# Kernel optimization log

Measured on AMD Instinct MI355X. Metric: run time of the kernel, lower is better.

## Reference

```python
import jax, jax.numpy as jnp
import numpy as np

N_NODES = 50000
N_EDGES = 800000
N_GRAPHS = 128
NEG_SLOPE = 0.2


def setup_inputs() -> dict:
    key = jax.random.key(0)
    ks = jax.random.split(key, 16)
    feature = jax.random.normal(ks[0], (N_NODES, 10), dtype=jnp.float32)
    src = jax.random.randint(ks[1], (N_EDGES,), 0, N_NODES, dtype=jnp.int32)
    dst = jax.random.randint(ks[2], (N_EDGES,), 0, N_NODES, dtype=jnp.int32)
    graph_ids = jnp.sort(jax.random.randint(ks[3], (N_NODES,), 0, N_GRAPHS, dtype=jnp.int32))
    s = 0.1
    W1 = jax.random.normal(ks[4], (10, 3 * 32), dtype=jnp.float32) * s
    al1 = jax.random.normal(ks[5], (3, 32), dtype=jnp.float32) * s
    ar1 = jax.random.normal(ks[6], (3, 32), dtype=jnp.float32) * s
    W2 = jax.random.normal(ks[7], (96, 3 * 64), dtype=jnp.float32) * s
    al2 = jax.random.normal(ks[8], (3, 64), dtype=jnp.float32) * s
    ar2 = jax.random.normal(ks[9], (3, 64), dtype=jnp.float32) * s
    d1_w = jax.random.normal(ks[10], (192, 64), dtype=jnp.float32) * s
    d1_b = jnp.zeros((64,), dtype=jnp.float32)
    d2_w = jax.random.normal(ks[11], (64, 1), dtype=jnp.float32) * s
    d2_b = jnp.zeros((1,), dtype=jnp.float32)
    return {"feature": feature, "src": src, "dst": dst, "graph_ids": graph_ids,
            "W1": W1, "al1": al1, "ar1": ar1, "W2": W2, "al2": al2, "ar2": ar2,
            "d1_w": d1_w, "d1_b": d1_b, "d2_w": d2_w, "d2_b": d2_b}


def _edge_softmax(e, dst, n_nodes):
    # e: [E, H] unnormalized logits; softmax over incoming edges of each dst node
    m = jax.ops.segment_max(e, dst, num_segments=n_nodes)  # [N, H]
    ex = jnp.exp(e - m[dst])
    s = jax.ops.segment_sum(ex, dst, num_segments=n_nodes)  # [N, H]
    return ex / (s[dst] + 1e-16)


def _gat_layer(x, W, al, ar, src, dst, n_nodes):
    H, D = al.shape
    z = (x @ W).reshape(n_nodes, H, D)                     # [N, H, D]
    el = jnp.einsum('nhd,hd->nh', z, al)                   # [N, H]
    er = jnp.einsum('nhd,hd->nh', z, ar)
    e = jax.nn.leaky_relu(el[src] + er[dst], NEG_SLOPE)    # [E, H]
    a = _edge_softmax(e, dst, n_nodes)                     # [E, H]
    msg = z[src] * a[:, :, None]                           # [E, H, D]
    out = jax.ops.segment_sum(msg, dst, num_segments=n_nodes)
    return out.reshape(n_nodes, H * D)


def reference(feature, src, dst, graph_ids, W1, al1, ar1, W2, al2, ar2, d1_w, d1_b, d2_w, d2_b):
    n = feature.shape[0]
    x1 = jax.nn.relu(_gat_layer(feature, W1, al1, ar1, src, dst, n))  # [N, 96]
    x2 = jax.nn.relu(_gat_layer(x1, W2, al2, ar2, src, dst, n))       # [N, 192]
    # AvgPooling: mean of node features per graph
    sums = jax.ops.segment_sum(x2, graph_ids, num_segments=N_GRAPHS)  # [G, 192]
    cnts = jax.ops.segment_sum(jnp.ones((n,), x2.dtype), graph_ids, num_segments=N_GRAPHS)
    pooled = sums / jnp.maximum(cnts, 1.0)[:, None]
    h = jax.nn.relu(pooled @ d1_w + d1_b)
    return h @ d2_w + d2_b  # [G, 1]
```

## Files before the change

kernel.cpp:

```cpp
#include <hip/hip_runtime.h>
#include <hip/hip_bf16.h>

#define NEG_SLOPE 0.2f

typedef __attribute__((ext_vector_type(8))) short short8v;
typedef __attribute__((ext_vector_type(4))) float f32x4;

__device__ __forceinline__ float wave_max64(float v) {
    for (int o = 32; o; o >>= 1) v = fmaxf(v, __shfl_xor(v, o));
    return v;
}
__device__ __forceinline__ float wave_sum64(float v) {
    for (int o = 32; o; o >>= 1) v += __shfl_xor(v, o);
    return v;
}
__device__ __forceinline__ unsigned short f2bf(float f) {
    unsigned int u = __float_as_uint(f);
    unsigned int r = (u + 0x7fffu + ((u >> 16) & 1u)) >> 16;
    return (unsigned short)r;
}
__device__ __forceinline__ float bf2f(unsigned short u) {
    return __uint_as_float(((unsigned int)u) << 16);
}


__global__ __launch_bounds__(256) void k_hist(const int* __restrict__ dst,
                                              int* __restrict__ deg,
                                              int* __restrict__ rank, int E) {
    int e = blockIdx.x * 256 + threadIdx.x;
    if (e < E) rank[e] = atomicAdd(&deg[dst[e]], 1);
}


__global__ __launch_bounds__(256) void k_scan1(const int* __restrict__ deg,
                                               int* __restrict__ bsum, int n) {
    int idx = blockIdx.x * 256 + threadIdx.x;
    int v = idx < n ? deg[idx] : 0;
    for (int o = 32; o; o >>= 1) v += __shfl_xor(v, o);
    __shared__ int ws[4];
    if ((threadIdx.x & 63) == 0) ws[threadIdx.x >> 6] = v;
    __syncthreads();
    if (threadIdx.x == 0) bsum[blockIdx.x] = ws[0] + ws[1] + ws[2] + ws[3];
}

__global__ __launch_bounds__(256) void k_scan2(const int* __restrict__ bsum,
                                               int* __restrict__ bpre,
                                               int* __restrict__ row_start,
                                               int nb, int n) {
    __shared__ int s[256];
    int t = threadIdx.x;
    int v = t < nb ? bsum[t] : 0;
    s[t] = v;
    __syncthreads();
    for (int o = 1; o < 256; o <<= 1) {
        int u = (t >= o) ? s[t - o] : 0;
        __syncthreads();
        s[t] += u;
        __syncthreads();
    }
    if (t < nb) bpre[t] = s[t] - v;
    if (t == 255) row_start[n] = s[255];
}

__global__ __launch_bounds__(256) void k_scan3(const int* __restrict__ deg,
                                               const int* __restrict__ bpre,
                                               int* __restrict__ row_start, int n) {
    int idx = blockIdx.x * 256 + threadIdx.x;
    int lane = threadIdx.x & 63;
    int w = threadIdx.x >> 6;
    int d = idx < n ? deg[idx] : 0;
    int x = d;
    for (int o = 1; o < 64; o <<= 1) {
        int u = __shfl_up(x, o);
        if (lane >= o) x += u;
    }
    __shared__ int ws[4];
    if (lane == 63) ws[w] = x;
    __syncthreads();
    int add = bpre[blockIdx.x];
    for (int i = 0; i < w; i++) add += ws[i];
    if (idx < n) row_start[idx] = add + x - d;
}


__global__ void k_scatter(const int* __restrict__ dst, const int* __restrict__ src,
                          const int* __restrict__ rank, const int* __restrict__ row_start,
                          int* __restrict__ ssrc, int E) {
    int e = blockIdx.x * blockDim.x + threadIdx.x;
    if (e < E) {
        int d = dst[e];
        ssrc[row_start[d] + rank[e]] = src[e];
    }
}


__global__ __launch_bounds__(256) void k_gemm1(const float* __restrict__ feat,
                                               const float* __restrict__ W1,
                                               const float* __restrict__ al,
                                               const float* __restrict__ ar,
                                               const float* __restrict__ W2,
                                               unsigned short* __restrict__ W2T,
                                               unsigned short* __restrict__ z1,
                                               float4* __restrict__ el1,
                                               float4* __restrict__ er1, int n) {
    for (int idx = blockIdx.x * 256 + threadIdx.x; idx < 96 * 192; idx += gridDim.x * 256) {
        int c = idx / 96, k = idx - c * 96;
        W2T[idx] = f2bf(W2[k * 192 + c]);
    }
    __shared__ float sW[960], sal[96], sar[96];
    for (int i = threadIdx.x; i < 960; i += 256) sW[i] = W1[i];
    for (int i = threadIdx.x; i < 96; i += 256) { sal[i] = al[i]; sar[i] = ar[i]; }
    __syncthreads();
    int nd = blockIdx.x * 256 + threadIdx.x;
    if (nd >= n) return;
    float x[10];
#pragma unroll
    for (int k = 0; k < 10; k++) x[k] = feat[(size_t)nd * 10 + k];
    float el[3] = {0.f, 0.f, 0.f}, er[3] = {0.f, 0.f, 0.f};
#pragma unroll
    for (int h = 0; h < 3; h++) {
#pragma unroll
        for (int d0 = 0; d0 < 32; d0 += 4) {
            ushort4 o;
            unsigned short* op = &o.x;
#pragma unroll
            for (int q = 0; q < 4; q++) {
                int c = h * 32 + d0 + q;
                float acc = 0.f;
#pragma unroll
                for (int k = 0; k < 10; k++) acc += x[k] * sW[k * 96 + c];
                op[q] = f2bf(acc);
                el[h] += acc * sal[c];
                er[h] += acc * sar[c];
            }
            *reinterpret_cast<ushort4*>(&z1[(size_t)nd * 96 + h * 32 + d0]) = o;
        }
    }
    el1[nd] = make_float4(el[0], el[1], el[2], 0.f);
    er1[nd] = make_float4(er[0], er[1], er[2], 0.f);
}


template <int D, int VW>
__global__ __launch_bounds__(256) void k_agg(const unsigned short* __restrict__ z,
                                             const float4* __restrict__ el,
                                             const float4* __restrict__ er,
                                             const int* __restrict__ row_start,
                                             const int* __restrict__ ssrc,
                                             unsigned short* __restrict__ xout, int n) {
    constexpr int H = 3;
    constexpr int HD = H * D;
    constexpr int NL = HD / VW;
    __shared__ float pl[4][272];
    int wid = (blockIdx.x * blockDim.x + threadIdx.x) >> 6;
    int lane = threadIdx.x & 63;
    int w = threadIdx.x >> 6;
    if (wid >= n) return;
    int s0 = row_start[wid];
    int deg = row_start[wid + 1] - s0;
    unsigned short* orow = xout + (size_t)wid * HD;
    if (deg <= 0) {
        if (lane < NL) {
            if constexpr (VW == 2)
                *reinterpret_cast<ushort2*>(orow + VW * lane) = make_ushort2(0, 0);
            else
                *reinterpret_cast<ushort4*>(orow + VW * lane) = make_ushort4(0, 0, 0, 0);
        }
        return;
    }
    float4 erv = er[wid];
    int hh = (VW * lane) / D;
    if (hh >= H) hh = H - 1;

    if (deg <= 64) {
        bool act = lane < deg;
        int sv = act ? ssrc[s0 + lane] : 0;
        float4 elv = el[sv];
        float v0 = elv.x + erv.x; v0 = v0 > 0.f ? v0 : NEG_SLOPE * v0;
        float v1 = elv.y + erv.y; v1 = v1 > 0.f ? v1 : NEG_SLOPE * v1;
        float v2 = elv.z + erv.z; v2 = v2 > 0.f ? v2 : NEG_SLOPE * v2;
        if (!act) { v0 = -3.402823466e38f; v1 = v0; v2 = v0; }
        float m0 = wave_max64(v0), m1 = wave_max64(v1), m2 = wave_max64(v2);
        float p0 = act ? __expf(v0 - m0) : 0.f;
        float p1 = act ? __expf(v1 - m1) : 0.f;
        float p2 = act ? __expf(v2 - m2) : 0.f;
        float i0 = 1.f / (wave_sum64(p0) + 1e-16f);
        float i1 = 1.f / (wave_sum64(p1) + 1e-16f);
        float i2 = 1.f / (wave_sum64(p2) + 1e-16f);
        pl[w][0 * 68 + lane] = p0 * i0;
        pl[w][1 * 68 + lane] = p1 * i1;
        pl[w][2 * 68 + lane] = p2 * i2;
        reinterpret_cast<int*>(&pl[w][204])[lane] = sv * HD;
        const float* pt = &pl[w][hh * 68];
        const int* zt = reinterpret_cast<const int*>(&pl[w][204]);

        int col = VW * (lane < NL ? lane : NL - 1);
        const unsigned short* zc = z + col;
        float acc0 = 0.f, acc1 = 0.f, acc2 = 0.f, acc3 = 0.f;
        int i = 0;
        for (; i + 8 <= deg; i += 8) {
            int zo[8];
#pragma unroll
            for (int j = 0; j < 8; j++) zo[j] = zt[i + j];
            if constexpr (VW == 2) {
                ushort2 r[8];
#pragma unroll
                for (int j = 0; j < 8; j++)
                    r[j] = *reinterpret_cast<const ushort2*>(zc + zo[j]);
#pragma unroll
                for (int j = 0; j < 8; j++) {
                    float a = pt[i + j];
                    acc0 += a * bf2f(r[j].x); acc1 += a * bf2f(r[j].y);
                }
            } else {
                ushort4 r[8];
#pragma unroll
                for (int j = 0; j < 8; j++)
                    r[j] = *reinterpret_cast<const ushort4*>(zc + zo[j]);
#pragma unroll
                for (int j = 0; j < 8; j++) {
                    float a = pt[i + j];
                    acc0 += a * bf2f(r[j].x); acc1 += a * bf2f(r[j].y);
                    acc2 += a * bf2f(r[j].z); acc3 += a * bf2f(r[j].w);
                }
            }
        }
        for (; i < deg; i++) {
            int zo = zt[i];
            float a = pt[i];
            if constexpr (VW == 2) {
                ushort2 zv = *reinterpret_cast<const ushort2*>(zc + zo);
                acc0 += a * bf2f(zv.x); acc1 += a * bf2f(zv.y);
            } else {
                ushort4 zv = *reinterpret_cast<const ushort4*>(zc + zo);
                acc0 += a * bf2f(zv.x); acc1 += a * bf2f(zv.y);
                acc2 += a * bf2f(zv.z); acc3 += a * bf2f(zv.w);
            }
        }
        if (lane < NL) {
            if constexpr (VW == 2) {
                ushort2 o2;
                o2.x = f2bf(fmaxf(acc0, 0.f)); o2.y = f2bf(fmaxf(acc1, 0.f));
                *reinterpret_cast<ushort2*>(orow + col) = o2;
            } else {
                ushort4 o4;
                o4.x = f2bf(fmaxf(acc0, 0.f)); o4.y = f2bf(fmaxf(acc1, 0.f));
                o4.z = f2bf(fmaxf(acc2, 0.f)); o4.w = f2bf(fmaxf(acc3, 0.f));
                *reinterpret_cast<ushort4*>(orow + col) = o4;
            }
        }
    } else {
        float ern[3] = {erv.x, erv.y, erv.z};
        float m[3] = {-3.402823466e38f, -3.402823466e38f, -3.402823466e38f};
        for (int i = lane; i < deg; i += 64) {
            int sv = ssrc[s0 + i];
            float4 elv = el[sv];
            float vv[3] = {elv.x, elv.y, elv.z};
#pragma unroll
            for (int h = 0; h < 3; h++) {
                float v = vv[h] + ern[h];
                v = v > 0.f ? v : NEG_SLOPE * v;
                m[h] = fmaxf(m[h], v);
            }
        }
#pragma unroll
        for (int h = 0; h < 3; h++) m[h] = wave_max64(m[h]);
        float s[3] = {0.f, 0.f, 0.f};
        for (int i = lane; i < deg; i += 64) {
            int sv = ssrc[s0 + i];
            float4 elv = el[sv];
            float vv[3] = {elv.x, elv.y, elv.z};
#pragma unroll
            for (int h = 0; h < 3; h++) {
                float v = vv[h] + ern[h];
                v = v > 0.f ? v : NEG_SLOPE * v;
                s[h] += __expf(v - m[h]);
            }
        }
#pragma unroll
        for (int h = 0; h < 3; h++) s[h] = 1.f / (wave_sum64(s[h]) + 1e-16f);
        constexpr int NC = (HD + 63) / 64;
        float acc[NC];
#pragma unroll
        for (int j = 0; j < NC; j++) acc[j] = 0.f;
        for (int i = 0; i < deg; i++) {
            int sv = ssrc[s0 + i];
            float4 elv = el[sv];
            float vv[3] = {elv.x, elv.y, elv.z};
            float a[3];
#pragma unroll
            for (int h = 0; h < 3; h++) {
                float v = vv[h] + ern[h];
                v = v > 0.f ? v : NEG_SLOPE * v;
                a[h] = __expf(v - m[h]) * s[h];
            }
            const unsigned short* zr = z + (size_t)sv * HD;
#pragma unroll
            for (int j = 0; j < NC; j++) {
                int c = lane + 64 * j;
                if (c < HD) acc[j] += a[c / D] * bf2f(zr[c]);
            }
        }
#pragma unroll
        for (int j = 0; j < NC; j++) {
            int c = lane + 64 * j;
            if (c < HD) orow[c] = f2bf(fmaxf(acc[j], 0.f));
        }
    }
}


__global__ __launch_bounds__(256) void k_gemm2(const unsigned short* __restrict__ x1,
                                               const unsigned short* __restrict__ W2T,
                                               const float* __restrict__ al,
                                               const float* __restrict__ ar,
                                               unsigned short* __restrict__ z2,
                                               float* __restrict__ el2,
                                               float* __restrict__ er2, int n) {
    int w = threadIdx.x >> 6;
    int l = threadIdx.x & 63;
    int q = l >> 4, c16 = l & 15;
    int Ra = blockIdx.x * 64 + w * 16 + c16;
    short8v afr[3];
    if (Ra < n) {
#pragma unroll
        for (int ks = 0; ks < 3; ks++)
            afr[ks] = *reinterpret_cast<const short8v*>(x1 + (size_t)Ra * 96 + ks * 32 + q * 8);
    } else {
#pragma unroll
        for (int ks = 0; ks < 3; ks++)
#pragma unroll
            for (int i = 0; i < 8; i++) afr[ks][i] = 0;
    }
    f32x4 acc[12];
#pragma unroll
    for (int t = 0; t < 12; t++)
#pragma unroll
        for (int r = 0; r < 4; r++) acc[t][r] = 0.f;
#pragma unroll
    for (int t = 0; t < 12; t++) {
        const unsigned short* bp = W2T + (t * 16 + c16) * 96 + q * 8;
#pragma unroll
        for (int ks = 0; ks < 3; ks++) {
            short8v bfr = *reinterpret_cast<const short8v*>(bp + ks * 32);
            acc[t] = __builtin_amdgcn_mfma_f32_16x16x32_bf16(afr[ks], bfr, acc[t], 0, 0, 0);
        }
    }
    int Rq = blockIdx.x * 64 + w * 16 + q * 4;
    float elp[4][3] = {}, erp[4][3] = {};
#pragma unroll
    for (int t = 0; t < 12; t++) {
        int h = t >> 2;
        float alv = al[t * 16 + c16];
        float arv = ar[t * 16 + c16];
#pragma unroll
        for (int r = 0; r < 4; r++) {
            float v = acc[t][r];
            elp[r][h] += v * alv;
            erp[r][h] += v * arv;
            if (Rq + r < n) z2[(size_t)(Rq + r) * 192 + t * 16 + c16] = f2bf(v);
        }
    }
#pragma unroll
    for (int r = 0; r < 4; r++)
#pragma unroll
        for (int h = 0; h < 3; h++)
#pragma unroll
            for (int o = 1; o < 16; o <<= 1) {
                elp[r][h] += __shfl_xor(elp[r][h], o);
                erp[r][h] += __shfl_xor(erp[r][h], o);
            }
    if (c16 == 0) {
#pragma unroll
        for (int r = 0; r < 4; r++)
            if (Rq + r < n) {
#pragma unroll
                for (int h = 0; h < 3; h++) {
                    el2[(Rq + r) * 4 + h] = elp[r][h];
                    er2[(Rq + r) * 4 + h] = erp[r][h];
                }
            }
    }
}


__global__ __launch_bounds__(192) void k_pool(const unsigned short* __restrict__ x2,
                                              const int* __restrict__ gid,
                                              float* __restrict__ gsum, int n) {
    int base = blockIdx.x * 32;
    if (base >= n) return;
    int end = base + 32; if (end > n) end = n;
    int c = threadIdx.x;
    float acc = 0.f;
    int gprev = gid[base];
    for (int i = base; i < end; i++) {
        int g = gid[i];
        if (g != gprev) {
            atomicAdd(&gsum[gprev * 192 + c], acc);
            acc = 0.f;
            gprev = g;
        }
        acc += bf2f(x2[(size_t)i * 192 + c]);
    }
    atomicAdd(&gsum[gprev * 192 + c], acc);
}


__global__ __launch_bounds__(64) void k_head(const float* __restrict__ gsum,
                                             const int* __restrict__ gid,
                                             const float* __restrict__ d1w,
                                             const float* __restrict__ d1b,
                                             const float* __restrict__ d2w,
                                             const float* __restrict__ d2b,
                                             float* __restrict__ out, int n, int G) {
    int g = blockIdx.x, j = threadIdx.x;
    int lo0 = 0, hi0 = n;
    while (lo0 < hi0) { int mid = (lo0 + hi0) >> 1; if (gid[mid] < g) lo0 = mid + 1; else hi0 = mid; }
    int lo1 = lo0, hi1 = n;
    while (lo1 < hi1) { int mid = (lo1 + hi1) >> 1; if (gid[mid] < g + 1) lo1 = mid + 1; else hi1 = mid; }
    float inv = 1.f / fmaxf((float)(lo1 - lo0), 1.f);
    float h = d1b[j];
    for (int k = 0; k < 192; k++) h += (gsum[g * 192 + k] * inv) * d1w[(size_t)k * 64 + j];
    h = fmaxf(h, 0.f);
    float v = h * d2w[j];
    for (int o = 32; o; o >>= 1) v += __shfl_xor(v, o);
    if (j == 0) out[g] = v + d2b[0];
}


extern "C" void kernel_launch(void* const* d_in, const int* in_sizes, int n_in,
                              void* d_out, int out_size, void* d_ws, size_t ws_size,
                              hipStream_t stream) {
    const float* feat = (const float*)d_in[0];
    const int* src = (const int*)d_in[1];
    const int* dst = (const int*)d_in[2];
    const int* gid = (const int*)d_in[3];
    const float* W1 = (const float*)d_in[4];
    const float* al1 = (const float*)d_in[5];
    const float* ar1 = (const float*)d_in[6];
    const float* W2 = (const float*)d_in[7];
    const float* al2 = (const float*)d_in[8];
    const float* ar2 = (const float*)d_in[9];
    const float* d1w = (const float*)d_in[10];
    const float* d1b = (const float*)d_in[11];
    const float* d2w = (const float*)d_in[12];
    const float* d2b = (const float*)d_in[13];
    float* out = (float*)d_out;
    const int N = in_sizes[0] / 10;
    const int E = in_sizes[1];
    const int G = out_size;
    const int NB = (N + 255) / 256;

    char* p = (char*)d_ws;
    auto take = [&](size_t bytes) -> char* {
        char* r = p;
        p += (bytes + 255) & ~(size_t)255;
        return r;
    };
    unsigned short* z1 = (unsigned short*)take((size_t)N * 96 * 2);
    unsigned short* x1 = (unsigned short*)take((size_t)N * 96 * 2);
    unsigned short* x2 = z1;
    unsigned short* z2 = (unsigned short*)take((size_t)N * 192 * 2);
    float4* el1 = (float4*)take((size_t)N * 16);
    float4* er1 = (float4*)take((size_t)N * 16);
    float* el2 = (float*)take((size_t)N * 16);
    float* er2 = (float*)take((size_t)N * 16);
    unsigned short* W2T = (unsigned short*)take((size_t)96 * 192 * 2);
    int* rank = (int*)take((size_t)E * 4);
    int* bsum = (int*)take((size_t)NB * 4);
    int* bpre = (int*)take((size_t)NB * 4);
    size_t zbytes = (size_t)N * 4 + (size_t)G * 192 * 4;
    int* deg = (int*)take(zbytes);
    float* gsum = (float*)(deg + N);
    int* row_start = (int*)take((size_t)(N + 1) * 4);
    int* ssrc = (int*)take((size_t)E * 4);

    hipMemsetAsync(deg, 0, zbytes, stream);

    k_hist<<<(E + 255) / 256, 256, 0, stream>>>(dst, deg, rank, E);
    k_gemm1<<<(N + 255) / 256, 256, 0, stream>>>(feat, W1, al1, ar1, W2, W2T,
                                                 z1, el1, er1, N);
    k_scan1<<<NB, 256, 0, stream>>>(deg, bsum, N);
    k_scan2<<<1, 256, 0, stream>>>(bsum, bpre, row_start, NB, N);
    k_scan3<<<NB, 256, 0, stream>>>(deg, bpre, row_start, N);
    k_scatter<<<(E + 255) / 256, 256, 0, stream>>>(dst, src, rank, row_start, ssrc, E);

    k_agg<32, 2><<<((size_t)N * 64 + 255) / 256, 256, 0, stream>>>(
        z1, el1, er1, row_start, ssrc, x1, N);
    k_gemm2<<<(N + 63) / 64, 256, 0, stream>>>(x1, W2T, al2, ar2, z2, el2, er2, N);
    k_agg<64, 4><<<((size_t)N * 64 + 255) / 256, 256, 0, stream>>>(
        z2, (const float4*)el2, (const float4*)er2, row_start, ssrc, x2, N);
    k_pool<<<(N + 31) / 32, 192, 0, stream>>>(x2, gid, gsum, N);
    k_head<<<G, 64, 0, stream>>>(gsum, gid, d1w, d1b, d2w, d2b, out, N, G);
}
```

Before: 286.8 us.

## Aggregate before projecting in both GAT layers and precompute attention vectors

Uses linearity to reorder each GAT layer: attention logits come from precomputed W·a vectors, so el/er no longer need the projected features. Raw input features (10 per node, per head) are aggregated first and then projected by W1. Layer 2 aggregates 96-wide x1 once per head into a 288-wide buffer and then runs a per-head MFMA GEMM. The aim is to shrink per-edge gather width, since layer 1 gathers 10 floats instead of 96 bf16. The cost is a larger intermediate (y2 at 288 wide) and an extra projection pass.

```diff
diff --git a/kernel.cpp b/kernel.cpp
--- a/kernel.cpp
+++ b/kernel.cpp
@@ -22,13 +22,38 @@
 __device__ __forceinline__ float bf2f(unsigned short u) {
     return __uint_as_float(((unsigned int)u) << 16);
 }
+__device__ __forceinline__ float bflo(unsigned int pk) {
+    return __uint_as_float(pk << 16);
+}
+__device__ __forceinline__ float bfhi(unsigned int pk) {
+    return __uint_as_float(pk & 0xFFFF0000u);
+}
 
 
 __global__ __launch_bounds__(256) void k_hist(const int* __restrict__ dst,
                                               int* __restrict__ deg,
-                                              int* __restrict__ rank, int E) {
-    int e = blockIdx.x * 256 + threadIdx.x;
-    if (e < E) rank[e] = atomicAdd(&deg[dst[e]], 1);
+                                              int* __restrict__ rank, int E,
+                                              const float* __restrict__ W2,
+                                              const float* __restrict__ al2,
+                                              const float* __restrict__ ar2,
+                                              unsigned short* __restrict__ W2T,
+                                              float* __restrict__ val2,
+                                              float* __restrict__ var2) {
+    int idx = blockIdx.x * 256 + threadIdx.x;
+    if (idx < 96 * 192) {
+        int c = idx / 96, k = idx - c * 96;
+        W2T[idx] = f2bf(W2[k * 192 + c]);
+    } else if (idx < 96 * 192 + 2 * 288) {
+        int t = idx - 96 * 192;
+        int which = t / 288;
+        int tt = t - which * 288;
+        int h = tt / 96, j = tt - h * 96;
+        const float* av = which ? ar2 : al2;
+        float a = 0.f;
+        for (int d = 0; d < 64; d++) a += W2[j * 192 + h * 64 + d] * av[h * 64 + d];
+        (which ? var2 : val2)[tt] = a;
+    }
+    if (idx < E) rank[idx] = atomicAdd(&deg[dst[idx]], 1);
 }
 
 
@@ -82,75 +107,60 @@
     if (idx < n) row_start[idx] = add + x - d;
 }
 
-
 __global__ void k_scatter(const int* __restrict__ dst, const int* __restrict__ src,
                           const int* __restrict__ rank, const int* __restrict__ row_start,
                           int* __restrict__ ssrc, int E) {
     int e = blockIdx.x * blockDim.x + threadIdx.x;
-    if (e < E) {
-        int d = dst[e];
-        ssrc[row_start[d] + rank[e]] = src[e];
-    }
-}
-
-
-__global__ __launch_bounds__(256) void k_gemm1(const float* __restrict__ feat,
-                                               const float* __restrict__ W1,
-                                               const float* __restrict__ al,
-                                               const float* __restrict__ ar,
-                                               const float* __restrict__ W2,
-                                               unsigned short* __restrict__ W2T,
-                                               unsigned short* __restrict__ z1,
-                                               float4* __restrict__ el1,
-                                               float4* __restrict__ er1, int n) {
-    for (int idx = blockIdx.x * 256 + threadIdx.x; idx < 96 * 192; idx += gridDim.x * 256) {
-        int c = idx / 96, k = idx - c * 96;
-        W2T[idx] = f2bf(W2[k * 192 + c]);
-    }
-    __shared__ float sW[960], sal[96], sar[96];
+    if (e < E) ssrc[row_start[dst[e]] + rank[e]] = src[e];
+}
+
+
+__global__ __launch_bounds__(256) void k_el1(const float* __restrict__ feat,
+                                             const float* __restrict__ W1,
+                                             const float* __restrict__ al,
+                                             const float* __restrict__ ar,
+                                             float4* __restrict__ el1,
+                                             float4* __restrict__ er1, int n) {
+    __shared__ float sW[960], sal[96], sar[96], sval[30], svar[30];
     for (int i = threadIdx.x; i < 960; i += 256) sW[i] = W1[i];
     for (int i = threadIdx.x; i < 96; i += 256) { sal[i] = al[i]; sar[i] = ar[i]; }
     __syncthreads();
-    int nd = blockIdx.x * 256 + threadIdx.x;
+    int t = threadIdx.x;
+    if (t < 30) {
+        int h = t / 10, k = t - h * 10;
+        float a = 0.f, b = 0.f;
+        for (int d = 0; d < 32; d++) {
+            float wv = sW[k * 96 + h * 32 + d];
+            a += wv * sal[h * 32 + d];
+            b += wv * sar[h * 32 + d];
+        }
+        sval[t] = a; svar[t] = b;
+    }
+    __syncthreads();
+    int nd = blockIdx.x * 256 + t;
     if (nd >= n) return;
     float x[10];
 #pragma unroll
     for (int k = 0; k < 10; k++) x[k] = feat[(size_t)nd * 10 + k];
-    float el[3] = {0.f, 0.f, 0.f}, er[3] = {0.f, 0.f, 0.f};
-#pragma unroll
-    for (int h = 0; h < 3; h++) {
-#pragma unroll
-        for (int d0 = 0; d0 < 32; d0 += 4) {
-            ushort4 o;
-            unsigned short* op = &o.x;
-#pragma unroll
-            for (int q = 0; q < 4; q++) {
-                int c = h * 32 + d0 + q;
-                float acc = 0.f;
-#pragma unroll
-                for (int k = 0; k < 10; k++) acc += x[k] * sW[k * 96 + c];
-                op[q] = f2bf(acc);
-                el[h] += acc * sal[c];
-                er[h] += acc * sar[c];
-            }
-            *reinterpret_cast<ushort4*>(&z1[(size_t)nd * 96 + h * 32 + d0]) = o;
-        }
-    }
+    float el[3] = {}, er[3] = {};
+#pragma unroll
+    for (int h = 0; h < 3; h++)
+#pragma unroll
+        for (int k = 0; k < 10; k++) {
+            el[h] += x[k] * sval[h * 10 + k];
+            er[h] += x[k] * svar[h * 10 + k];
+        }
     el1[nd] = make_float4(el[0], el[1], el[2], 0.f);
     er1[nd] = make_float4(er[0], er[1], er[2], 0.f);
 }
 
 
-template <int D, int VW>
-__global__ __launch_bounds__(256) void k_agg(const unsigned short* __restrict__ z,
-                                             const float4* __restrict__ el,
-                                             const float4* __restrict__ er,
-                                             const int* __restrict__ row_start,
-                                             const int* __restrict__ ssrc,
-                                             unsigned short* __restrict__ xout, int n) {
-    constexpr int H = 3;
-    constexpr int HD = H * D;
-    constexpr int NL = HD / VW;
+__global__ __launch_bounds__(256) void k_agg1(const float* __restrict__ feat,
+                                              const float4* __restrict__ el,
+                                              const float4* __restrict__ er,
+                                              const int* __restrict__ row_start,
+                                              const int* __restrict__ ssrc,
+                                              float* __restrict__ y1, int n) {
     __shared__ float pl[4][272];
     int wid = (blockIdx.x * blockDim.x + threadIdx.x) >> 6;
     int lane = threadIdx.x & 63;
@@ -158,19 +168,14 @@
     if (wid >= n) return;
     int s0 = row_start[wid];
     int deg = row_start[wid + 1] - s0;
-    unsigned short* orow = xout + (size_t)wid * HD;
     if (deg <= 0) {
-        if (lane < NL) {
-            if constexpr (VW == 2)
-                *reinterpret_cast<ushort2*>(orow + VW * lane) = make_ushort2(0, 0);
-            else
-                *reinterpret_cast<ushort4*>(orow + VW * lane) = make_ushort4(0, 0, 0, 0);
-        }
+        if (lane < 30) y1[(size_t)wid * 30 + lane] = 0.f;
         return;
     }
     float4 erv = er[wid];
-    int hh = (VW * lane) / D;
-    if (hh >= H) hh = H - 1;
+    int ll = lane & 31, hf = lane >> 5;
+    int h = ll / 10, k = ll - (ll / 10) * 10;
+    if (ll >= 30) { h = 2; k = 9; }
 
     if (deg <= 64) {
         bool act = lane < deg;
@@ -190,65 +195,33 @@
         pl[w][0 * 68 + lane] = p0 * i0;
         pl[w][1 * 68 + lane] = p1 * i1;
         pl[w][2 * 68 + lane] = p2 * i2;
-        reinterpret_cast<int*>(&pl[w][204])[lane] = sv * HD;
-        const float* pt = &pl[w][hh * 68];
+        reinterpret_cast<int*>(&pl[w][204])[lane] = sv * 10;
+        const float* pt = &pl[w][h * 68];
         const int* zt = reinterpret_cast<const int*>(&pl[w][204]);
 
-        int col = VW * (lane < NL ? lane : NL - 1);
-        const unsigned short* zc = z + col;
-        float acc0 = 0.f, acc1 = 0.f, acc2 = 0.f, acc3 = 0.f;
+        float acc = 0.f;
         int i = 0;
         for (; i + 8 <= deg; i += 8) {
-            int zo[8];
-#pragma unroll
-            for (int j = 0; j < 8; j++) zo[j] = zt[i + j];
-            if constexpr (VW == 2) {
-                ushort2 r[8];
-#pragma unroll
-                for (int j = 0; j < 8; j++)
-                    r[j] = *reinterpret_cast<const ushort2*>(zc + zo[j]);
-#pragma unroll
-                for (int j = 0; j < 8; j++) {
-                    float a = pt[i + j];
-                    acc0 += a * bf2f(r[j].x); acc1 += a * bf2f(r[j].y);
-                }
-            } else {
-                ushort4 r[8];
-#pragma unroll
-                for (int j = 0; j < 8; j++)
-                    r[j] = *reinterpret_cast<const ushort4*>(zc + zo[j]);
-#pragma unroll
-                for (int j = 0; j < 8; j++) {
-                    float a = pt[i + j];
-                    acc0 += a * bf2f(r[j].x); acc1 += a * bf2f(r[j].y);
-                    acc2 += a * bf2f(r[j].z); acc3 += a * bf2f(r[j].w);
-                }
-            }
-        }
-        for (; i < deg; i++) {
-            int zo = zt[i];
-            float a = pt[i];
-            if constexpr (VW == 2) {
-                ushort2 zv = *reinterpret_cast<const ushort2*>(zc + zo);
-                acc0 += a * bf2f(zv.x); acc1 += a * bf2f(zv.y);
-            } else {
-                ushort4 zv = *reinterpret_cast<const ushort4*>(zc + zo);
-                acc0 += a * bf2f(zv.x); acc1 += a * bf2f(zv.y);
-                acc2 += a * bf2f(zv.z); acc3 += a * bf2f(zv.w);
-            }
-        }
-        if (lane < NL) {
-            if constexpr (VW == 2) {
-                ushort2 o2;
-                o2.x = f2bf(fmaxf(acc0, 0.f)); o2.y = f2bf(fmaxf(acc1, 0.f));
-                *reinterpret_cast<ushort2*>(orow + col) = o2;
-            } else {
-                ushort4 o4;
-                o4.x = f2bf(fmaxf(acc0, 0.f)); o4.y = f2bf(fmaxf(acc1, 0.f));
-                o4.z = f2bf(fmaxf(acc2, 0.f)); o4.w = f2bf(fmaxf(acc3, 0.f));
-                *reinterpret_cast<ushort4*>(orow + col) = o4;
-            }
-        }
+            float vv[4], aa[4];
+#pragma unroll
+            for (int j = 0; j < 4; j++) {
+                int e = i + 2 * j + hf;
+                int zo = zt[e];
+                vv[j] = feat[zo + k];
+                aa[j] = pt[e];
+            }
+#pragma unroll
+            for (int j = 0; j < 4; j++) acc += aa[j] * vv[j];
+        }
+        for (; i < deg; i += 2) {
+            int e = i + hf;
+            if (e < deg) {
+                int zo = zt[e];
+                acc += pt[e] * feat[zo + k];
+            }
+        }
+        acc += __shfl_xor(acc, 32);
+        if (lane < 30) y1[(size_t)wid * 30 + lane] = acc;
     } else {
         float ern[3] = {erv.x, erv.y, erv.z};
         float m[3] = {-3.402823466e38f, -3.402823466e38f, -3.402823466e38f};
@@ -257,66 +230,228 @@
             float4 elv = el[sv];
             float vv[3] = {elv.x, elv.y, elv.z};
 #pragma unroll
-            for (int h = 0; h < 3; h++) {
-                float v = vv[h] + ern[h];
+            for (int hh = 0; hh < 3; hh++) {
+                float v = vv[hh] + ern[hh];
                 v = v > 0.f ? v : NEG_SLOPE * v;
-                m[h] = fmaxf(m[h], v);
-            }
-        }
-#pragma unroll
-        for (int h = 0; h < 3; h++) m[h] = wave_max64(m[h]);
-        float s[3] = {0.f, 0.f, 0.f};
+                m[hh] = fmaxf(m[hh], v);
+            }
+        }
+#pragma unroll
+        for (int hh = 0; hh < 3; hh++) m[hh] = wave_max64(m[hh]);
+        float s[3] = {};
         for (int i = lane; i < deg; i += 64) {
             int sv = ssrc[s0 + i];
             float4 elv = el[sv];
             float vv[3] = {elv.x, elv.y, elv.z};
 #pragma unroll
-            for (int h = 0; h < 3; h++) {
-                float v = vv[h] + ern[h];
+            for (int hh = 0; hh < 3; hh++) {
+                float v = vv[hh] + ern[hh];
                 v = v > 0.f ? v : NEG_SLOPE * v;
-                s[h] += __expf(v - m[h]);
-            }
-        }
-#pragma unroll
-        for (int h = 0; h < 3; h++) s[h] = 1.f / (wave_sum64(s[h]) + 1e-16f);
-        constexpr int NC = (HD + 63) / 64;
-        float acc[NC];
-#pragma unroll
-        for (int j = 0; j < NC; j++) acc[j] = 0.f;
+                s[hh] += __expf(v - m[hh]);
+            }
+        }
+#pragma unroll
+        for (int hh = 0; hh < 3; hh++) s[hh] = 1.f / (wave_sum64(s[hh]) + 1e-16f);
+        float acc = 0.f;
+        for (int i = 0; i < deg; i++) {
+            int sv = ssrc[s0 + i];
+            float4 elv = el[sv];
+            float vv[3] = {elv.x, elv.y, elv.z};
+            float v = vv[h] + ern[h];
+            v = v > 0.f ? v : NEG_SLOPE * v;
+            float a = __expf(v - m[h]) * s[h];
+            acc += a * feat[sv * 10 + k];
+        }
+        if (lane < 30) y1[(size_t)wid * 30 + lane] = acc;
+    }
+}
+
+
+__global__ __launch_bounds__(256) void k_xform1(const float* __restrict__ y1,
+                                                const float* __restrict__ W1,
+                                                const float* __restrict__ val2,
+                                                const float* __restrict__ var2,
+                                                unsigned short* __restrict__ x1,
+                                                float4* __restrict__ el2,
+                                                float4* __restrict__ er2, int n) {
+    __shared__ float sW[960], sv2[288], sr2[288];
+    for (int i = threadIdx.x; i < 960; i += 256) sW[i] = W1[i];
+    for (int i = threadIdx.x; i < 288; i += 256) { sv2[i] = val2[i]; sr2[i] = var2[i]; }
+    __syncthreads();
+    int nd = blockIdx.x * 256 + threadIdx.x;
+    if (nd >= n) return;
+    float y[30];
+#pragma unroll
+    for (int i = 0; i < 30; i++) y[i] = y1[(size_t)nd * 30 + i];
+    float el[3] = {}, er[3] = {};
+#pragma unroll
+    for (int h = 0; h < 3; h++) {
+#pragma unroll
+        for (int d0 = 0; d0 < 32; d0 += 4) {
+            ushort4 o;
+            unsigned short* op = &o.x;
+#pragma unroll
+            for (int q = 0; q < 4; q++) {
+                int c = h * 32 + d0 + q;
+                float acc = 0.f;
+#pragma unroll
+                for (int k = 0; k < 10; k++) acc += y[h * 10 + k] * sW[k * 96 + c];
+                float r = fmaxf(acc, 0.f);
+                op[q] = f2bf(r);
+#pragma unroll
+                for (int hh = 0; hh < 3; hh++) {
+                    el[hh] += r * sv2[hh * 96 + c];
+                    er[hh] += r * sr2[hh * 96 + c];
+                }
+            }
+            *reinterpret_cast<ushort4*>(&x1[(size_t)nd * 96 + h * 32 + d0]) = o;
+        }
+    }
+    el2[nd] = make_float4(el[0], el[1], el[2], 0.f);
+    er2[nd] = make_float4(er[0], er[1], er[2], 0.f);
+}
+
+
+__global__ __launch_bounds__(256) void k_agg2(const unsigned short* __restrict__ x1,
+                                              const float4* __restrict__ el,
+                                              const float4* __restrict__ er,
+                                              const int* __restrict__ row_start,
+                                              const int* __restrict__ ssrc,
+                                              unsigned short* __restrict__ y2, int n) {
+    __shared__ float pl[4][272];
+    int wid = (blockIdx.x * blockDim.x + threadIdx.x) >> 6;
+    int lane = threadIdx.x & 63;
+    int w = threadIdx.x >> 6;
+    if (wid >= n) return;
+    int s0 = row_start[wid];
+    int deg = row_start[wid + 1] - s0;
+    int c0 = lane < 48 ? lane * 2 : 0;
+    if (deg <= 0) {
+        if (lane < 48) {
+#pragma unroll
+            for (int h = 0; h < 3; h++)
+                *reinterpret_cast<ushort2*>(&y2[(size_t)wid * 288 + h * 96 + c0]) =
+                    make_ushort2(0, 0);
+        }
+        return;
+    }
+    float4 erv = er[wid];
+    float acc[3][2] = {};
+
+    if (deg <= 64) {
+        bool act = lane < deg;
+        int sv = act ? ssrc[s0 + lane] : 0;
+        float4 elv = el[sv];
+        float v0 = elv.x + erv.x; v0 = v0 > 0.f ? v0 : NEG_SLOPE * v0;
+        float v1 = elv.y + erv.y; v1 = v1 > 0.f ? v1 : NEG_SLOPE * v1;
+        float v2 = elv.z + erv.z; v2 = v2 > 0.f ? v2 : NEG_SLOPE * v2;
+        if (!act) { v0 = -3.402823466e38f; v1 = v0; v2 = v0; }
+        float m0 = wave_max64(v0), m1 = wave_max64(v1), m2 = wave_max64(v2);
+        float p0 = act ? __expf(v0 - m0) : 0.f;
+        float p1 = act ? __expf(v1 - m1) : 0.f;
+        float p2 = act ? __expf(v2 - m2) : 0.f;
+        float i0 = 1.f / (wave_sum64(p0) + 1e-16f);
+        float i1 = 1.f / (wave_sum64(p1) + 1e-16f);
+        float i2 = 1.f / (wave_sum64(p2) + 1e-16f);
+        pl[w][0 * 68 + lane] = p0 * i0;
+        pl[w][1 * 68 + lane] = p1 * i1;
+        pl[w][2 * 68 + lane] = p2 * i2;
+        reinterpret_cast<int*>(&pl[w][204])[lane] = sv * 96;
+        const float* pt0 = &pl[w][0];
+        const float* pt1 = &pl[w][68];
+        const float* pt2 = &pl[w][136];
+        const int* zt = reinterpret_cast<const int*>(&pl[w][204]);
+        const unsigned short* zc = x1 + c0;
+
+        int i = 0;
+        for (; i + 8 <= deg; i += 8) {
+            int zo[8];
+#pragma unroll
+            for (int j = 0; j < 8; j++) zo[j] = zt[i + j];
+            unsigned int r[8];
+#pragma unroll
+            for (int j = 0; j < 8; j++)
+                r[j] = *reinterpret_cast<const unsigned int*>(zc + zo[j]);
+#pragma unroll
+            for (int j = 0; j < 8; j++) {
+                float lo = bflo(r[j]), hi = bfhi(r[j]);
+                float a0 = pt0[i + j], a1 = pt1[i + j], a2 = pt2[i + j];
+                acc[0][0] += a0 * lo; acc[0][1] += a0 * hi;
+                acc[1][0] += a1 * lo; acc[1][1] += a1 * hi;
+                acc[2][0] += a2 * lo; acc[2][1] += a2 * hi;
+            }
+        }
+        for (; i < deg; i++) {
+            unsigned int r = *reinterpret_cast<const unsigned int*>(zc + zt[i]);
+            float lo = bflo(r), hi = bfhi(r);
+            float a0 = pt0[i], a1 = pt1[i], a2 = pt2[i];
+            acc[0][0] += a0 * lo; acc[0][1] += a0 * hi;
+            acc[1][0] += a1 * lo; acc[1][1] += a1 * hi;
+            acc[2][0] += a2 * lo; acc[2][1] += a2 * hi;
+        }
+    } else {
+        float ern[3] = {erv.x, erv.y, erv.z};
+        float m[3] = {-3.402823466e38f, -3.402823466e38f, -3.402823466e38f};
+        for (int i = lane; i < deg; i += 64) {
+            int sv = ssrc[s0 + i];
+            float4 elv = el[sv];
+            float vv[3] = {elv.x, elv.y, elv.z};
+#pragma unroll
+            for (int hh = 0; hh < 3; hh++) {
+                float v = vv[hh] + ern[hh];
+                v = v > 0.f ? v : NEG_SLOPE * v;
+                m[hh] = fmaxf(m[hh], v);
+            }
+        }
+#pragma unroll
+        for (int hh = 0; hh < 3; hh++) m[hh] = wave_max64(m[hh]);
+        float s[3] = {};
+        for (int i = lane; i < deg; i += 64) {
+            int sv = ssrc[s0 + i];
+            float4 elv = el[sv];
+            float vv[3] = {elv.x, elv.y, elv.z};
+#pragma unroll
+            for (int hh = 0; hh < 3; hh++) {
+                float v = vv[hh] + ern[hh];
+                v = v > 0.f ? v : NEG_SLOPE * v;
+                s[hh] += __expf(v - m[hh]);
+            }
+        }
+#pragma unroll
+        for (int hh = 0; hh < 3; hh++) s[hh] = 1.f / (wave_sum64(s[hh]) + 1e-16f);
         for (int i = 0; i < deg; i++) {
             int sv = ssrc[s0 + i];
             float4 elv = el[sv];
             float vv[3] = {elv.x, elv.y, elv.z};
             float a[3];
 #pragma unroll
-            for (int h = 0; h < 3; h++) {
-                float v = vv[h] + ern[h];
+            for (int hh = 0; hh < 3; hh++) {
+                float v = vv[hh] + ern[hh];
                 v = v > 0.f ? v : NEG_SLOPE * v;
-                a[h] = __expf(v - m[h]) * s[h];
-            }
-            const unsigned short* zr = z + (size_t)sv * HD;
-#pragma unroll
-            for (int j = 0; j < NC; j++) {
-                int c = lane + 64 * j;
-                if (c < HD) acc[j] += a[c / D] * bf2f(zr[c]);
-            }
-        }
-#pragma unroll
-        for (int j = 0; j < NC; j++) {
-            int c = lane + 64 * j;
-            if (c < HD) orow[c] = f2bf(fmaxf(acc[j], 0.f));
-        }
-    }
-}
-
-
-__global__ __launch_bounds__(256) void k_gemm2(const unsigned short* __restrict__ x1,
-                                               const unsigned short* __restrict__ W2T,
-                                               const float* __restrict__ al,
-                                               const float* __restrict__ ar,
-                                               unsigned short* __restrict__ z2,
-                                               float* __restrict__ el2,
-                                               float* __restrict__ er2, int n) {
+                a[hh] = __expf(v - m[hh]) * s[hh];
+            }
+            unsigned int r = *reinterpret_cast<const unsigned int*>(x1 + sv * 96 + c0);
+            float lo = bflo(r), hi = bfhi(r);
+            acc[0][0] += a[0] * lo; acc[0][1] += a[0] * hi;
+            acc[1][0] += a[1] * lo; acc[1][1] += a[1] * hi;
+            acc[2][0] += a[2] * lo; acc[2][1] += a[2] * hi;
+        }
+    }
+    if (lane < 48) {
+#pragma unroll
+        for (int h = 0; h < 3; h++) {
+            ushort2 o2;
+            o2.x = f2bf(acc[h][0]); o2.y = f2bf(acc[h][1]);
+            *reinterpret_cast<ushort2*>(&y2[(size_t)wid * 288 + h * 96 + c0]) = o2;
+        }
+    }
+}
+
+
+__global__ __launch_bounds__(256) void k_xform2(const unsigned short* __restrict__ y2,
+                                                const unsigned short* __restrict__ W2T,
+                                                unsigned short* __restrict__ x2, int n) {
+    int h = blockIdx.y;
     int w = threadIdx.x >> 6;
     int l = threadIdx.x & 63;
     int q = l >> 4, c16 = l & 15;
@@ -325,21 +460,22 @@
     if (Ra < n) {
 #pragma unroll
         for (int ks = 0; ks < 3; ks++)
-            afr[ks] = *reinterpret_cast<const short8v*>(x1 + (size_t)Ra * 96 + ks * 32 + q * 8);
+            afr[ks] = *reinterpret_cast<const short8v*>(y2 + (size_t)Ra * 288 + h * 96 +
+                                                        ks * 32 + q * 8);
     } else {
 #pragma unroll
         for (int ks = 0; ks < 3; ks++)
 #pragma unroll
             for (int i = 0; i < 8; i++) afr[ks][i] = 0;
     }
-    f32x4 acc[12];
-#pragma unroll
-    for (int t = 0; t < 12; t++)
+    f32x4 acc[4];
+#pragma unroll
+    for (int t = 0; t < 4; t++)
 #pragma unroll
         for (int r = 0; r < 4; r++) acc[t][r] = 0.f;
 #pragma unroll
-    for (int t = 0; t < 12; t++) {
-        const unsigned short* bp = W2T + (t * 16 + c16) * 96 + q * 8;
+    for (int t = 0; t < 4; t++) {
+        const unsigned short* bp = W2T + (size_t)(h * 64 + t * 16 + c16) * 96 + q * 8;
 #pragma unroll
         for (int ks = 0; ks < 3; ks++) {
             short8v bfr = *reinterpret_cast<const short8v*>(bp + ks * 32);
@@ -347,39 +483,14 @@
         }
     }
     int Rq = blockIdx.x * 64 + w * 16 + q * 4;
-    float elp[4][3] = {}, erp[4][3] = {};
-#pragma unroll
-    for (int t = 0; t < 12; t++) {
-        int h = t >> 2;
-        float alv = al[t * 16 + c16];
-        float arv = ar[t * 16 + c16];
+#pragma unroll
+    for (int t = 0; t < 4; t++) {
 #pragma unroll
         for (int r = 0; r < 4; r++) {
-            float v = acc[t][r];
-            elp[r][h] += v * alv;
-            erp[r][h] += v * arv;
-            if (Rq + r < n) z2[(size_t)(Rq + r) * 192 + t * 16 + c16] = f2bf(v);
-        }
-    }
-#pragma unroll
-    for (int r = 0; r < 4; r++)
-#pragma unroll
-        for (int h = 0; h < 3; h++)
-#pragma unroll
-            for (int o = 1; o < 16; o <<= 1) {
-                elp[r][h] += __shfl_xor(elp[r][h], o);
-                erp[r][h] += __shfl_xor(erp[r][h], o);
-            }
-    if (c16 == 0) {
-#pragma unroll
-        for (int r = 0; r < 4; r++)
-            if (Rq + r < n) {
-#pragma unroll
-                for (int h = 0; h < 3; h++) {
-                    el2[(Rq + r) * 4 + h] = elp[r][h];
-                    er2[(Rq + r) * 4 + h] = erp[r][h];
-                }
-            }
+            if (Rq + r < n)
+                x2[(size_t)(Rq + r) * 192 + h * 64 + t * 16 + c16] =
+                    f2bf(fmaxf(acc[t][r], 0.f));
+        }
     }
 }
 
@@ -457,15 +568,17 @@
         p += (bytes + 255) & ~(size_t)255;
         return r;
     };
-    unsigned short* z1 = (unsigned short*)take((size_t)N * 96 * 2);
+    float* y1 = (float*)take((size_t)N * 30 * 4);
     unsigned short* x1 = (unsigned short*)take((size_t)N * 96 * 2);
-    unsigned short* x2 = z1;
-    unsigned short* z2 = (unsigned short*)take((size_t)N * 192 * 2);
+    unsigned short* y2 = (unsigned short*)take((size_t)N * 288 * 2);
+    unsigned short* x2 = (unsigned short*)take((size_t)N * 192 * 2);
     float4* el1 = (float4*)take((size_t)N * 16);
     float4* er1 = (float4*)take((size_t)N * 16);
-    float* el2 = (float*)take((size_t)N * 16);
-    float* er2 = (float*)take((size_t)N * 16);
+    float4* el2 = (float4*)take((size_t)N * 16);
+    float4* er2 = (float4*)take((size_t)N * 16);
     unsigned short* W2T = (unsigned short*)take((size_t)96 * 192 * 2);
+    float* val2 = (float*)take((size_t)288 * 4);
+    float* var2 = (float*)take((size_t)288 * 4);
     int* rank = (int*)take((size_t)E * 4);
     int* bsum = (int*)take((size_t)NB * 4);
     int* bpre = (int*)take((size_t)NB * 4);
@@ -477,19 +590,20 @@
 
     hipMemsetAsync(deg, 0, zbytes, stream);
 
-    k_hist<<<(E + 255) / 256, 256, 0, stream>>>(dst, deg, rank, E);
-    k_gemm1<<<(N + 255) / 256, 256, 0, stream>>>(feat, W1, al1, ar1, W2, W2T,
-                                                 z1, el1, er1, N);
+    k_hist<<<(E + 255) / 256, 256, 0, stream>>>(dst, deg, rank, E, W2, al2, ar2,
+                                                W2T, val2, var2);
+    k_el1<<<NB, 256, 0, stream>>>(feat, W1, al1, ar1, el1, er1, N);
     k_scan1<<<NB, 256, 0, stream>>>(deg, bsum, N);
     k_scan2<<<1, 256, 0, stream>>>(bsum, bpre, row_start, NB, N);
     k_scan3<<<NB, 256, 0, stream>>>(deg, bpre, row_start, N);
     k_scatter<<<(E + 255) / 256, 256, 0, stream>>>(dst, src, rank, row_start, ssrc, E);
 
-    k_agg<32, 2><<<((size_t)N * 64 + 255) / 256, 256, 0, stream>>>(
-        z1, el1, er1, row_start, ssrc, x1, N);
-    k_gemm2<<<(N + 63) / 64, 256, 0, stream>>>(x1, W2T, al2, ar2, z2, el2, er2, N);
-    k_agg<64, 4><<<((size_t)N * 64 + 255) / 256, 256, 0, stream>>>(
-        z2, (const float4*)el2, (const float4*)er2, row_start, ssrc, x2, N);
+    k_agg1<<<((size_t)N * 64 + 255) / 256, 256, 0, stream>>>(feat, el1, er1, row_start,
+                                                             ssrc, y1, N);
+    k_xform1<<<NB, 256, 0, stream>>>(y1, W1, val2, var2, x1, el2, er2, N);
+    k_agg2<<<((size_t)N * 64 + 255) / 256, 256, 0, stream>>>(x1, el2, er2, row_start,
+                                                             ssrc, y2, N);
+    k_xform2<<<dim3((N + 63) / 64, 3), 256, 0, stream>>>(y2, W2T, x2, N);
     k_pool<<<(N + 31) / 32, 192, 0, stream>>>(x2, gid, gsum, N);
     k_head<<<G, 64, 0, stream>>>(gsum, gid, d1w, d1b, d2w, d2b, out, N, G);
 }
```

New measurement: 276.3 us. -3.6%, faster.
